# Optimization experiments

Hardware: AMD Instinct MI355X
Metric: run time of the kernel (lower is better)

## Reference

```python
import jax, jax.numpy as jnp
import numpy as np

HEADS = 8


def setup_inputs() -> dict:
    key = jax.random.key(0)
    ks = jax.random.split(key, 5)
    B, C, H, W = 2, 256, 48, 48
    s = 0.02
    return {
        "ct": jax.random.normal(ks[0], (B, C, H, W), jnp.float32),
        "us": jax.random.normal(ks[1], (B, C, H, W), jnp.float32),
        "w_qkv_ct": jax.random.normal(ks[2], (3 * C, C), jnp.float32) * s,
        "w_qkv_us": jax.random.normal(ks[3], (3 * C, C), jnp.float32) * s,
        "w_proj": jax.random.normal(ks[4], (C, 2 * C), jnp.float32) * s,
        "b_proj": jnp.zeros((C,), jnp.float32),
    }


def _heads_view(x, B, H, W):
    # [B, C, H, W] -> [B, heads, HW, dh]
    C = x.shape[1]
    return x.reshape(B, HEADS, C // HEADS, H * W).transpose(0, 1, 3, 2)


def _cross_attn(q, k, v, scale):
    # q,k,v: [B, heads, HW, dh]
    attn = jax.nn.softmax(jnp.einsum("bhnd,bhmd->bhnm", q, k) * scale, axis=-1)
    return jnp.einsum("bhnm,bhmd->bhnd", attn, v)


def reference(ct, us, w_qkv_ct, w_qkv_us, w_proj, b_proj):
    B, C, H, W = ct.shape
    dh = C // HEADS
    scale = dh ** (-0.5)

    # 1x1 convs as channel GEMMs
    qkv1 = jnp.einsum("oc,bchw->bohw", w_qkv_ct, ct)
    qkv2 = jnp.einsum("oc,bchw->bohw", w_qkv_us, us)
    q1, k1, v1 = jnp.split(qkv1, 3, axis=1)
    q2, k2, v2 = jnp.split(qkv2, 3, axis=1)

    # CT queries attend to US keys/values
    o1 = _cross_attn(_heads_view(q1, B, H, W), _heads_view(k2, B, H, W),
                     _heads_view(v2, B, H, W), scale)
    # US queries attend to CT keys/values
    o2 = _cross_attn(_heads_view(q2, B, H, W), _heads_view(k1, B, H, W),
                     _heads_view(v1, B, H, W), scale)

    # [B, heads, HW, dh] -> [B, C, H, W]
    out1 = o1.transpose(0, 1, 3, 2).reshape(B, C, H, W)
    out2 = o2.transpose(0, 1, 3, 2).reshape(B, C, H, W)

    fused = jnp.concatenate([ct + out1, us + out2], axis=1)
    return jnp.einsum("oc,bchw->bohw", w_proj, fused) + b_proj[None, :, None, None]
```

## Files before the change

### kernel.cpp

```cpp
#include <hip/hip_runtime.h>
#include <hip/hip_bf16.h>
#include <hip/hip_cooperative_groups.h>
#include <math.h>

namespace cg = cooperative_groups;

#define HW   2304
#define CCH  256

#define QSCALE 0.25504368686637270f

typedef short short8 __attribute__((ext_vector_type(8)));
typedef float f32x4  __attribute__((ext_vector_type(4)));

__device__ inline unsigned short f2bf(float f) {
    union { float f; unsigned u; } v; v.f = f;
    unsigned r = v.u + 0x7FFF + ((v.u >> 16) & 1);
    return (unsigned short)(r >> 16);
}
__device__ inline unsigned pkbf2(float a, float b) {
    float2 f; f.x = a; f.y = b;
    union { __hip_bfloat162 h; unsigned u; } c;
    c.h = __float22bfloat162_rn(f);
    return c.u;
}
__device__ inline unsigned pktrunc(float a, float b) {
    return __builtin_amdgcn_perm(__builtin_bit_cast(unsigned, b),
                                 __builtin_bit_cast(unsigned, a), 0x07060302u);
}

__device__ __forceinline__ int xswz(int i, int chunk) {
    return (i & 7) * chunk + (i >> 3);
}


__device__ __forceinline__ void prep_unit(
    int u, int t,
    const float* __restrict__ ct, const float* __restrict__ us,
    const float* __restrict__ w1, const float* __restrict__ w2,
    const float* __restrict__ w3,
    unsigned short* __restrict__ xT,
    unsigned short* __restrict__ wb1, unsigned short* __restrict__ wb2,
    unsigned short* __restrict__ w3b,
    unsigned short* __restrict__ Ts )
{
    if (u >= 576) {
        const int v_ = u - 576;
        int z, base;
        if (v_ < 192)      { z = 0; base = v_ * 1024; }
        else if (v_ < 384) { z = 1; base = (v_ - 192) * 1024; }
        else               { z = 2; base = (v_ - 384) * 1024; }
        const float* s = (z == 0) ? w1 : (z == 1) ? w2 : w3;
        unsigned short* d = (z == 0) ? wb1 : (z == 1) ? wb2 : w3b;
        const int i = base + t * 4;
        const float4 v4 = *(const float4*)&s[i];
        const float sc = (z < 2 && i < 65536) ? QSCALE : 1.f;
        uint2 p; p.x = pkbf2(v4.x * sc, v4.y * sc); p.y = pkbf2(v4.z * sc, v4.w * sc);
        *(uint2*)&d[i] = p;
        return;
    }
    const int pt = u % 36, rest = u / 36, ctile = rest & 3, z = rest >> 2;
    const float* __restrict__ src = ((z >> 1) ? us : ct) + (size_t)(z & 1) * CCH * HW;
    unsigned short* __restrict__ dst = xT + (size_t)z * HW * 256;
    const int p0 = pt * 64, c0 = ctile * 64;
    __syncthreads();
#pragma unroll
    for (int r = 0; r < 4; r++) {
        const int c = (t >> 4) + 16 * r;
        const float4 v4 = *(const float4*)&src[(size_t)(c0 + c) * HW + p0 + (t & 15) * 4];
        Ts[((t & 15) * 4 + 0) * 72 + c] = f2bf(v4.x);
        Ts[((t & 15) * 4 + 1) * 72 + c] = f2bf(v4.y);
        Ts[((t & 15) * 4 + 2) * 72 + c] = f2bf(v4.z);
        Ts[((t & 15) * 4 + 3) * 72 + c] = f2bf(v4.w);
    }
    __syncthreads();
    const int p = t >> 2, c8 = (t & 3) * 16;
    const short8 a  = *(const short8*)&Ts[p * 72 + c8];
    const short8 b8 = *(const short8*)&Ts[p * 72 + c8 + 8];
    *(short8*)&dst[(size_t)(p0 + p) * 256 + c0 + c8]     = a;
    *(short8*)&dst[(size_t)(p0 + p) * 256 + c0 + c8 + 8] = b8;
}

__device__ __forceinline__ void qkv_unit(
    int ptile, int otile, int z, int t,
    const unsigned short* __restrict__ xT,
    const unsigned short* __restrict__ wb1, const unsigned short* __restrict__ wb2,
    unsigned short* __restrict__ qkvT1, unsigned short* __restrict__ qkvT2,
    unsigned short* __restrict__ vdm1,  unsigned short* __restrict__ vdm2,
    unsigned short* __restrict__ Ws, unsigned short* __restrict__ Xs)
{
    const int inp = z >> 1, b = z & 1;
    const unsigned short* __restrict__ X = xT + (size_t)(inp * 2 + b) * HW * 256;
    const unsigned short* __restrict__ W = inp ? wb2 : wb1;
    unsigned short* __restrict__ qT = (inp ? qkvT2 : qkvT1) + (size_t)b * HW * 512;
    unsigned short* __restrict__ vd = (inp ? vdm2 : vdm1) + (size_t)b * CCH * HW;
    const int p0 = ptile * 64, o0 = otile * 64;
    const int w = t >> 6, lane = t & 63, quad = lane >> 4, m = lane & 15;
    const int sr = t >> 3, sc = t & 7;

    f32x4 acc[4] = {{0,0,0,0},{0,0,0,0},{0,0,0,0},{0,0,0,0}};

    short8 wv0 = *(const short8*)&W[(size_t)(o0 + sr) * 256 + sc * 8];
    short8 wv1 = *(const short8*)&W[(size_t)(o0 + 32 + sr) * 256 + sc * 8];
    short8 xv0 = *(const short8*)&X[(size_t)(p0 + sr) * 256 + sc * 8];
    short8 xv1 = *(const short8*)&X[(size_t)(p0 + 32 + sr) * 256 + sc * 8];

    for (int k0 = 0; k0 < 256; k0 += 64) {
        __syncthreads();
        *(short8*)&Ws[sr * 72 + sc * 8] = wv0;
        *(short8*)&Ws[(32 + sr) * 72 + sc * 8] = wv1;
        *(short8*)&Xs[sr * 72 + sc * 8] = xv0;
        *(short8*)&Xs[(32 + sr) * 72 + sc * 8] = xv1;
        __syncthreads();
        const int kn = k0 + 64;
        if (kn < 256) {
            wv0 = *(const short8*)&W[(size_t)(o0 + sr) * 256 + kn + sc * 8];
            wv1 = *(const short8*)&W[(size_t)(o0 + 32 + sr) * 256 + kn + sc * 8];
            xv0 = *(const short8*)&X[(size_t)(p0 + sr) * 256 + kn + sc * 8];
            xv1 = *(const short8*)&X[(size_t)(p0 + 32 + sr) * 256 + kn + sc * 8];
        }
#pragma unroll
        for (int kc2 = 0; kc2 < 2; kc2++) {
            const short8 af = *(const short8*)&Ws[(w * 16 + m) * 72 + kc2 * 32 + quad * 8];
#pragma unroll
            for (int pg = 0; pg < 4; pg++) {
                const short8 bf = *(const short8*)&Xs[(pg * 16 + m) * 72 + kc2 * 32 + quad * 8];
                acc[pg] = __builtin_amdgcn_mfma_f32_16x16x32_bf16(af, bf, acc[pg], 0, 0, 0);
            }
        }
    }
    __syncthreads();
    if (o0 < 512) {
#pragma unroll
        for (int pg = 0; pg < 4; pg++) {
            uint2 pk; pk.x = pkbf2(acc[pg][0], acc[pg][1]); pk.y = pkbf2(acc[pg][2], acc[pg][3]);
            *(uint2*)&Ws[(pg * 16 + m) * 72 + w * 16 + quad * 4] = pk;
        }
        __syncthreads();
        const int pr = t >> 2, cc = t & 3;
        const uint4 d0 = *(const uint4*)&Ws[pr * 72 + cc * 16];
        const uint4 d1 = *(const uint4*)&Ws[pr * 72 + cc * 16 + 8];
        *(uint4*)&qT[(size_t)(p0 + pr) * 512 + o0 + cc * 16]     = d0;
        *(uint4*)&qT[(size_t)(p0 + pr) * 512 + o0 + cc * 16 + 8] = d1;
    } else {
#pragma unroll
        for (int pg = 0; pg < 4; pg++)
#pragma unroll
            for (int r = 0; r < 4; r++)
                Ws[(w * 16 + quad * 4 + r) * 72 + pg * 16 + m] = f2bf(acc[pg][r]);
        __syncthreads();
        const int dr = t >> 2, cc = t & 3;
        const uint4 d0 = *(const uint4*)&Ws[dr * 72 + cc * 16];
        const uint4 d1 = *(const uint4*)&Ws[dr * 72 + cc * 16 + 8];
        *(uint4*)&vd[(size_t)(o0 - 512 + dr) * HW + p0 + cc * 16]     = d0;
        *(uint4*)&vd[(size_t)(o0 - 512 + dr) * HW + p0 + cc * 16 + 8] = d1;
    }
    __syncthreads();
}

__device__ __forceinline__ void attn_unit(
    int ptile, int dir, int b, int h, int t,
    const unsigned short* __restrict__ qkvT1, const unsigned short* __restrict__ qkvT2,
    const unsigned short* __restrict__ vdm1,  const unsigned short* __restrict__ vdm2,
    const float* __restrict__ ct, const float* __restrict__ us,
    unsigned short* __restrict__ fusedT,
    unsigned short* __restrict__ Ks , unsigned short* __restrict__ Vs )
{
    const unsigned short* __restrict__ Qt = (dir ? qkvT2 : qkvT1) + (size_t)b * HW * 512;
    const unsigned short* __restrict__ Kt = (dir ? qkvT1 : qkvT2) + (size_t)b * HW * 512
                                            + 256 + h * 32;
    const unsigned short* __restrict__ Vd = (dir ? vdm1 : vdm2) + ((size_t)b * CCH + h * 32) * HW;
    const float* __restrict__ src = (dir ? us : ct) + ((size_t)b * CCH + h * 32) * HW;

    const int w = t >> 6, lane = t & 63, quad = lane >> 4, m = lane & 15;
    const int kj0 = t >> 2, kcs = t & 3;
    const int pcK = kcs ^ (((kj0 >> 1) & 1) | (((kj0 >> 3) & 1) << 1));
    const int vr0 = t >> 4, vcs = t & 15;
    const int g2m = ((m >> 1) & 1) | (((m >> 2) & 1) << 1);
    const unsigned short* __restrict__ ksb =
        &Ks[((m >> 2) * 8 + (m & 3)) * 32 + (quad ^ g2m) * 8];
    const unsigned short* __restrict__ vsb = &Vs[m * 136 + quad * 8];
    const short ONE = (short)0x3F80;
    const short8 ones = {ONE,ONE,ONE,ONE,ONE,ONE,ONE,ONE};

    const int pq = ptile * 64 + w * 16 + m;
    const short8 qf = *(const short8*)&Qt[(size_t)pq * 512 + h * 32 + quad * 8];

    f32x4 acc0 = {0,0,0,0}, acc1 = {0,0,0,0}, accl = {0,0,0,0};

    short8 ka = *(const short8*)&Kt[(size_t)kj0 * 512 + kcs * 8];
    short8 kb = *(const short8*)&Kt[(size_t)(kj0 + 64) * 512 + kcs * 8];
    short8 va = *(const short8*)&Vd[(size_t)vr0 * HW + vcs * 8];
    short8 vb = *(const short8*)&Vd[(size_t)(vr0 + 16) * HW + vcs * 8];

    for (int j0 = 0; j0 < HW; j0 += 128) {
        __syncthreads();
        *(short8*)&Ks[kj0 * 32 + pcK * 8] = ka;
        *(short8*)&Ks[(kj0 + 64) * 32 + pcK * 8] = kb;
        *(short8*)&Vs[vr0 * 136 + vcs * 8] = va;
        *(short8*)&Vs[(vr0 + 16) * 136 + vcs * 8] = vb;
        __syncthreads();

        const int jn = j0 + 128;
        if (jn < HW) {
            ka = *(const short8*)&Kt[(size_t)(jn + kj0) * 512 + kcs * 8];
            kb = *(const short8*)&Kt[(size_t)(jn + kj0 + 64) * 512 + kcs * 8];
            va = *(const short8*)&Vd[(size_t)vr0 * HW + jn + vcs * 8];
            vb = *(const short8*)&Vd[(size_t)(vr0 + 16) * HW + jn + vcs * 8];
        }

        uint4 pw4[4];
#pragma unroll
        for (int f = 0; f < 8; f++) {
            const short8 kf = *(const short8*)(ksb + ((f >> 1) * 32 + (f & 1) * 4) * 32);
            const f32x4 z = {0,0,0,0};
            const f32x4 S = __builtin_amdgcn_mfma_f32_16x16x32_bf16(kf, qf, z, 0, 0, 0);
            const float e0 = __builtin_amdgcn_exp2f(S[0]);
            const float e1 = __builtin_amdgcn_exp2f(S[1]);
            const float e2 = __builtin_amdgcn_exp2f(S[2]);
            const float e3 = __builtin_amdgcn_exp2f(S[3]);
            if ((f & 1) == 0) { pw4[f >> 1].x = pktrunc(e0, e1); pw4[f >> 1].y = pktrunc(e2, e3); }
            else              { pw4[f >> 1].z = pktrunc(e0, e1); pw4[f >> 1].w = pktrunc(e2, e3); }
        }
#pragma unroll
        for (int kt = 0; kt < 4; kt++) {
            const short8 pf = __builtin_bit_cast(short8, pw4[kt]);
            const short8 vf0 = *(const short8*)(vsb + kt * 32);
            const short8 vf1 = *(const short8*)(vsb + 16 * 136 + kt * 32);
            acc0 = __builtin_amdgcn_mfma_f32_16x16x32_bf16(vf0, pf, acc0, 0, 0, 0);
            acc1 = __builtin_amdgcn_mfma_f32_16x16x32_bf16(vf1, pf, acc1, 0, 0, 0);
            accl = __builtin_amdgcn_mfma_f32_16x16x32_bf16(ones, pf, accl, 0, 0, 0);
        }
    }

    const float inv = 1.f / accl[0];
    const int cb = dir * 256 + h * 32, d0 = quad * 4;
    unsigned short* __restrict__ fT = fusedT + ((size_t)b * HW + pq) * 512 + cb + d0;
    uint2 s0, s1;
    s0.x = pkbf2(acc0[0] * inv + src[(size_t)(d0 + 0) * HW + pq],
                 acc0[1] * inv + src[(size_t)(d0 + 1) * HW + pq]);
    s0.y = pkbf2(acc0[2] * inv + src[(size_t)(d0 + 2) * HW + pq],
                 acc0[3] * inv + src[(size_t)(d0 + 3) * HW + pq]);
    s1.x = pkbf2(acc1[0] * inv + src[(size_t)(16 + d0 + 0) * HW + pq],
                 acc1[1] * inv + src[(size_t)(16 + d0 + 1) * HW + pq]);
    s1.y = pkbf2(acc1[2] * inv + src[(size_t)(16 + d0 + 2) * HW + pq],
                 acc1[3] * inv + src[(size_t)(16 + d0 + 3) * HW + pq]);
    *(uint2*)&fT[0]  = s0;
    *(uint2*)&fT[16] = s1;
    __syncthreads();
}

__device__ __forceinline__ void proj_unit(
    int ptile, int otile, int t,
    const unsigned short* __restrict__ w3b, const unsigned short* __restrict__ fusedT,
    const float* __restrict__ bias, float* __restrict__ out,
    unsigned short* __restrict__ Ws, unsigned short* __restrict__ Xs)
{
    const int p0 = ptile * 64, o0 = otile * 64;
    const int w = t >> 6, lane = t & 63, quad = lane >> 4, m = lane & 15;
    const int sr = t >> 3, sc = t & 7;

    f32x4 acc[4] = {{0,0,0,0},{0,0,0,0},{0,0,0,0},{0,0,0,0}};

    short8 wv0 = *(const short8*)&w3b[(size_t)(o0 + sr) * 512 + sc * 8];
    short8 wv1 = *(const short8*)&w3b[(size_t)(o0 + 32 + sr) * 512 + sc * 8];
    short8 xv0 = *(const short8*)&fusedT[(size_t)(p0 + sr) * 512 + sc * 8];
    short8 xv1 = *(const short8*)&fusedT[(size_t)(p0 + 32 + sr) * 512 + sc * 8];

    for (int k0 = 0; k0 < 512; k0 += 64) {
        __syncthreads();
        *(short8*)&Ws[sr * 72 + sc * 8] = wv0;
        *(short8*)&Ws[(32 + sr) * 72 + sc * 8] = wv1;
        *(short8*)&Xs[sr * 72 + sc * 8] = xv0;
        *(short8*)&Xs[(32 + sr) * 72 + sc * 8] = xv1;
        __syncthreads();
        const int kn = k0 + 64;
        if (kn < 512) {
            wv0 = *(const short8*)&w3b[(size_t)(o0 + sr) * 512 + kn + sc * 8];
            wv1 = *(const short8*)&w3b[(size_t)(o0 + 32 + sr) * 512 + kn + sc * 8];
            xv0 = *(const short8*)&fusedT[(size_t)(p0 + sr) * 512 + kn + sc * 8];
            xv1 = *(const short8*)&fusedT[(size_t)(p0 + 32 + sr) * 512 + kn + sc * 8];
        }
#pragma unroll
        for (int kc2 = 0; kc2 < 2; kc2++) {
            const short8 af = *(const short8*)&Ws[(w * 16 + m) * 72 + kc2 * 32 + quad * 8];
#pragma unroll
            for (int pg = 0; pg < 4; pg++) {
                const short8 bf = *(const short8*)&Xs[(pg * 16 + m) * 72 + kc2 * 32 + quad * 8];
                acc[pg] = __builtin_amdgcn_mfma_f32_16x16x32_bf16(af, bf, acc[pg], 0, 0, 0);
            }
        }
    }
    const int b = (p0 >= HW) ? 1 : 0;
    const int pl0 = p0 - b * HW;
    float* __restrict__ ob = out + (size_t)b * CCH * HW;
    float b4[4];
#pragma unroll
    for (int r = 0; r < 4; r++) b4[r] = bias[o0 + w * 16 + quad * 4 + r];
#pragma unroll
    for (int pg = 0; pg < 4; pg++)
#pragma unroll
        for (int r = 0; r < 4; r++)
            ob[(size_t)(o0 + w * 16 + quad * 4 + r) * HW + pl0 + pg * 16 + m]
                = acc[pg][r] + b4[r];
}

__global__ __launch_bounds__(256, 5) void fused_k(
    const float* __restrict__ ct, const float* __restrict__ us,
    const float* __restrict__ w1, const float* __restrict__ w2,
    const float* __restrict__ w3, const float* __restrict__ bias,
    float* __restrict__ out,
    unsigned short* __restrict__ xT,
    unsigned short* __restrict__ wb1, unsigned short* __restrict__ wb2,
    unsigned short* __restrict__ w3b,
    unsigned short* __restrict__ qkvT1, unsigned short* __restrict__ qkvT2,
    unsigned short* __restrict__ vdm1,  unsigned short* __restrict__ vdm2,
    unsigned short* __restrict__ fusedT)
{
    cg::grid_group grid = cg::this_grid();
    __shared__ __align__(16) unsigned short smem[9216];
    const int t = threadIdx.x, nb = gridDim.x;

    for (int u = blockIdx.x; u < 1088; u += nb)
        prep_unit(u, t, ct, us, w1, w2, w3, xT, wb1, wb2, w3b, smem);
    __threadfence();
    grid.sync();

    for (int i = blockIdx.x; i < 1728; i += nb) {
        const int u = xswz(i, 216);
        const int ptile = u % 36, rest = u / 36;
        qkv_unit(ptile, rest % 12, rest / 12, t, xT, wb1, wb2,
                 qkvT1, qkvT2, vdm1, vdm2, smem, smem + 4608);
    }
    __threadfence();
    grid.sync();

    {
        const int u = xswz(blockIdx.x, 144);
        const int ptile = u % 36, rest = u / 36;
        attn_unit(ptile, rest >> 4, (rest >> 3) & 1, rest & 7, t,
                  qkvT1, qkvT2, vdm1, vdm2, ct, us, fusedT, smem, smem + 4096);
    }
    __threadfence();
    grid.sync();

    if (blockIdx.x < 288) {
        const int u = xswz(blockIdx.x, 36);
        proj_unit(u % 72, u / 72, t, w3b, fusedT, bias, out,
                  smem, smem + 4608);
    }
}

__global__ __launch_bounds__(256, 4) void prep_k(
    const float* __restrict__ ct, const float* __restrict__ us,
    const float* __restrict__ w1, const float* __restrict__ w2,
    const float* __restrict__ w3,
    unsigned short* __restrict__ xT,
    unsigned short* __restrict__ b1, unsigned short* __restrict__ b2,
    unsigned short* __restrict__ b3)
{
    __shared__ __align__(16) unsigned short Ts[64 * 72];
    prep_unit(blockIdx.x, threadIdx.x, ct, us, w1, w2, w3, xT, b1, b2, b3, Ts);
}

__global__ __launch_bounds__(256, 4) void qkv_k(
    const unsigned short* __restrict__ xT,
    const unsigned short* __restrict__ wb1, const unsigned short* __restrict__ wb2,
    unsigned short* __restrict__ qkvT1, unsigned short* __restrict__ qkvT2,
    unsigned short* __restrict__ vdm1,  unsigned short* __restrict__ vdm2)
{
    __shared__ __align__(16) unsigned short Ws[64 * 72];
    __shared__ __align__(16) unsigned short Xs[64 * 72];
    qkv_unit(blockIdx.x, blockIdx.y, blockIdx.z, threadIdx.x,
             xT, wb1, wb2, qkvT1, qkvT2, vdm1, vdm2, Ws, Xs);
}

__global__ __launch_bounds__(256, 5) void attn_k(
    const unsigned short* __restrict__ qkvT1, const unsigned short* __restrict__ qkvT2,
    const unsigned short* __restrict__ vdm1,  const unsigned short* __restrict__ vdm2,
    const float* __restrict__ ct, const float* __restrict__ us,
    unsigned short* __restrict__ fusedT)
{
    __shared__ __align__(16) unsigned short Ks[128 * 32];
    __shared__ __align__(16) unsigned short Vs[32 * 136];
    attn_unit(blockIdx.x, blockIdx.z, blockIdx.y >> 3, blockIdx.y & 7, threadIdx.x,
              qkvT1, qkvT2, vdm1, vdm2, ct, us, fusedT, Ks, Vs);
}

__global__ __launch_bounds__(256, 4) void proj_k(
    const unsigned short* __restrict__ w3b, const unsigned short* __restrict__ fusedT,
    const float* __restrict__ bias, float* __restrict__ out)
{
    __shared__ __align__(16) unsigned short Ws[64 * 72];
    __shared__ __align__(16) unsigned short Xs[64 * 72];
    proj_unit(blockIdx.x, blockIdx.y, threadIdx.x, w3b, fusedT, bias, out, Ws, Xs);
}

extern "C" void kernel_launch(void* const* d_in, const int* in_sizes, int n_in,
                              void* d_out, int out_size, void* d_ws, size_t ws_size,
                              hipStream_t stream)
{
    const float* ct       = (const float*)d_in[0];
    const float* us       = (const float*)d_in[1];
    const float* w_qkv_ct = (const float*)d_in[2];
    const float* w_qkv_us = (const float*)d_in[3];
    const float* w_proj   = (const float*)d_in[4];
    const float* b_proj   = (const float*)d_in[5];
    float* out = (float*)d_out;

    unsigned short* wb1   = (unsigned short*)d_ws;
    unsigned short* wb2   = wb1 + (size_t)768 * 256;
    unsigned short* w3b   = wb2 + (size_t)768 * 256;
    unsigned short* xT    = w3b + (size_t)256 * 512;
    unsigned short* qkvT1 = xT    + (size_t)4 * HW * 256;
    unsigned short* qkvT2 = qkvT1 + (size_t)2 * HW * 512;
    unsigned short* vdm1  = qkvT2 + (size_t)2 * HW * 512;
    unsigned short* vdm2  = vdm1  + (size_t)2 * CCH * HW;
    unsigned short* fusedT= vdm2  + (size_t)2 * CCH * HW;

    int dev = 0, coop = 0, occ = 0;
    bool did_coop = false;
    if (hipGetDevice(&dev) == hipSuccess &&
        hipDeviceGetAttribute(&coop, hipDeviceAttributeCooperativeLaunch, dev) == hipSuccess &&
        coop &&
        hipOccupancyMaxActiveBlocksPerMultiprocessor(&occ, fused_k, 256, 0) == hipSuccess &&
        occ >= 5)
    {
        void* args[] = {
            (void*)&ct, (void*)&us, (void*)&w_qkv_ct, (void*)&w_qkv_us,
            (void*)&w_proj, (void*)&b_proj, (void*)&out,
            (void*)&xT, (void*)&wb1, (void*)&wb2, (void*)&w3b,
            (void*)&qkvT1, (void*)&qkvT2, (void*)&vdm1, (void*)&vdm2, (void*)&fusedT
        };
        did_coop = (hipLaunchCooperativeKernel((const void*)fused_k, dim3(1152), dim3(256),
                                               args, 0, stream) == hipSuccess);
    }
    if (!did_coop) {
        prep_k<<<dim3(1088), 256, 0, stream>>>(ct, us, w_qkv_ct, w_qkv_us, w_proj,
                                               xT, wb1, wb2, w3b);
        qkv_k <<<dim3(36, 12, 4), 256, 0, stream>>>(xT, wb1, wb2, qkvT1, qkvT2, vdm1, vdm2);
        attn_k<<<dim3(36, 16, 2), 256, 0, stream>>>(qkvT1, qkvT2, vdm1, vdm2, ct, us, fusedT);
        proj_k<<<dim3(72, 4), 256, 0, stream>>>(w3b, fusedT, b_proj, out);
    }
}
```

Measured before the change: 126.0 us.

## Process two query tiles per attention wave and swizzle prep transpose LDS

```diff
diff --git a/kernel.cpp b/kernel.cpp
--- a/kernel.cpp
+++ b/kernel.cpp
@@ -63,20 +63,23 @@
     const float* __restrict__ src = ((z >> 1) ? us : ct) + (size_t)(z & 1) * CCH * HW;
     unsigned short* __restrict__ dst = xT + (size_t)z * HW * 256;
     const int p0 = pt * 64, c0 = ctile * 64;
+    const int m = t & 15, ms = (m & 7) << 3;
     __syncthreads();
 #pragma unroll
     for (int r = 0; r < 4; r++) {
         const int c = (t >> 4) + 16 * r;
-        const float4 v4 = *(const float4*)&src[(size_t)(c0 + c) * HW + p0 + (t & 15) * 4];
-        Ts[((t & 15) * 4 + 0) * 72 + c] = f2bf(v4.x);
-        Ts[((t & 15) * 4 + 1) * 72 + c] = f2bf(v4.y);
-        Ts[((t & 15) * 4 + 2) * 72 + c] = f2bf(v4.z);
-        Ts[((t & 15) * 4 + 3) * 72 + c] = f2bf(v4.w);
+        const float4 v4 = *(const float4*)&src[(size_t)(c0 + c) * HW + p0 + m * 4];
+        const int cs = c ^ ms;
+        Ts[(m * 4 + 0) * 72 + cs] = f2bf(v4.x);
+        Ts[(m * 4 + 1) * 72 + cs] = f2bf(v4.y);
+        Ts[(m * 4 + 2) * 72 + cs] = f2bf(v4.z);
+        Ts[(m * 4 + 3) * 72 + cs] = f2bf(v4.w);
     }
     __syncthreads();
     const int p = t >> 2, c8 = (t & 3) * 16;
-    const short8 a  = *(const short8*)&Ts[p * 72 + c8];
-    const short8 b8 = *(const short8*)&Ts[p * 72 + c8 + 8];
+    const int es = ((p >> 2) & 7) << 3;
+    const short8 a  = *(const short8*)&Ts[p * 72 + (c8 ^ es)];
+    const short8 b8 = *(const short8*)&Ts[p * 72 + ((c8 + 8) ^ es)];
     *(short8*)&dst[(size_t)(p0 + p) * 256 + c0 + c8]     = a;
     *(short8*)&dst[(size_t)(p0 + p) * 256 + c0 + c8 + 8] = b8;
 }
@@ -183,10 +186,12 @@
     const short ONE = (short)0x3F80;
     const short8 ones = {ONE,ONE,ONE,ONE,ONE,ONE,ONE,ONE};
 
-    const int pq = ptile * 64 + w * 16 + m;
-    const short8 qf = *(const short8*)&Qt[(size_t)pq * 512 + h * 32 + quad * 8];
-
-    f32x4 acc0 = {0,0,0,0}, acc1 = {0,0,0,0}, accl = {0,0,0,0};
+    const int pqA = ptile * 128 + w * 32 + m;
+    const short8 qfA = *(const short8*)&Qt[(size_t)pqA * 512 + h * 32 + quad * 8];
+    const short8 qfB = *(const short8*)&Qt[(size_t)(pqA + 16) * 512 + h * 32 + quad * 8];
+
+    f32x4 acc0A = {0,0,0,0}, acc1A = {0,0,0,0}, acclA = {0,0,0,0};
+    f32x4 acc0B = {0,0,0,0}, acc1B = {0,0,0,0}, acclB = {0,0,0,0};
 
     short8 ka = *(const short8*)&Kt[(size_t)kj0 * 512 + kcs * 8];
     short8 kb = *(const short8*)&Kt[(size_t)(kj0 + 64) * 512 + kcs * 8];
@@ -209,44 +214,76 @@
             vb = *(const short8*)&Vd[(size_t)(vr0 + 16) * HW + jn + vcs * 8];
         }
 
-        uint4 pw4[4];
+        uint4 pwA[4], pwB[4];
 #pragma unroll
         for (int f = 0; f < 8; f++) {
             const short8 kf = *(const short8*)(ksb + ((f >> 1) * 32 + (f & 1) * 4) * 32);
             const f32x4 z = {0,0,0,0};
-            const f32x4 S = __builtin_amdgcn_mfma_f32_16x16x32_bf16(kf, qf, z, 0, 0, 0);
-            const float e0 = __builtin_amdgcn_exp2f(S[0]);
-            const float e1 = __builtin_amdgcn_exp2f(S[1]);
-            const float e2 = __builtin_amdgcn_exp2f(S[2]);
-            const float e3 = __builtin_amdgcn_exp2f(S[3]);
-            if ((f & 1) == 0) { pw4[f >> 1].x = pktrunc(e0, e1); pw4[f >> 1].y = pktrunc(e2, e3); }
-            else              { pw4[f >> 1].z = pktrunc(e0, e1); pw4[f >> 1].w = pktrunc(e2, e3); }
+            const f32x4 SA = __builtin_amdgcn_mfma_f32_16x16x32_bf16(kf, qfA, z, 0, 0, 0);
+            const f32x4 SB = __builtin_amdgcn_mfma_f32_16x16x32_bf16(kf, qfB, z, 0, 0, 0);
+            const float a0 = __builtin_amdgcn_exp2f(SA[0]);
+            const float a1 = __builtin_amdgcn_exp2f(SA[1]);
+            const float a2 = __builtin_amdgcn_exp2f(SA[2]);
+            const float a3 = __builtin_amdgcn_exp2f(SA[3]);
+            const float b0 = __builtin_amdgcn_exp2f(SB[0]);
+            const float b1 = __builtin_amdgcn_exp2f(SB[1]);
+            const float b2 = __builtin_amdgcn_exp2f(SB[2]);
+            const float b3 = __builtin_amdgcn_exp2f(SB[3]);
+            if ((f & 1) == 0) {
+                pwA[f >> 1].x = pktrunc(a0, a1); pwA[f >> 1].y = pktrunc(a2, a3);
+                pwB[f >> 1].x = pktrunc(b0, b1); pwB[f >> 1].y = pktrunc(b2, b3);
+            } else {
+                pwA[f >> 1].z = pktrunc(a0, a1); pwA[f >> 1].w = pktrunc(a2, a3);
+                pwB[f >> 1].z = pktrunc(b0, b1); pwB[f >> 1].w = pktrunc(b2, b3);
+            }
         }
 #pragma unroll
         for (int kt = 0; kt < 4; kt++) {
-            const short8 pf = __builtin_bit_cast(short8, pw4[kt]);
+            const short8 pfA = __builtin_bit_cast(short8, pwA[kt]);
+            const short8 pfB = __builtin_bit_cast(short8, pwB[kt]);
             const short8 vf0 = *(const short8*)(vsb + kt * 32);
             const short8 vf1 = *(const short8*)(vsb + 16 * 136 + kt * 32);
-            acc0 = __builtin_amdgcn_mfma_f32_16x16x32_bf16(vf0, pf, acc0, 0, 0, 0);
-            acc1 = __builtin_amdgcn_mfma_f32_16x16x32_bf16(vf1, pf, acc1, 0, 0, 0);
-            accl = __builtin_amdgcn_mfma_f32_16x16x32_bf16(ones, pf, accl, 0, 0, 0);
-        }
-    }
-
-    const float inv = 1.f / accl[0];
+            acc0A = __builtin_amdgcn_mfma_f32_16x16x32_bf16(vf0, pfA, acc0A, 0, 0, 0);
+            acc1A = __builtin_amdgcn_mfma_f32_16x16x32_bf16(vf1, pfA, acc1A, 0, 0, 0);
+            acclA = __builtin_amdgcn_mfma_f32_16x16x32_bf16(ones, pfA, acclA, 0, 0, 0);
+            acc0B = __builtin_amdgcn_mfma_f32_16x16x32_bf16(vf0, pfB, acc0B, 0, 0, 0);
+            acc1B = __builtin_amdgcn_mfma_f32_16x16x32_bf16(vf1, pfB, acc1B, 0, 0, 0);
+            acclB = __builtin_amdgcn_mfma_f32_16x16x32_bf16(ones, pfB, acclB, 0, 0, 0);
+        }
+    }
+
     const int cb = dir * 256 + h * 32, d0 = quad * 4;
-    unsigned short* __restrict__ fT = fusedT + ((size_t)b * HW + pq) * 512 + cb + d0;
-    uint2 s0, s1;
-    s0.x = pkbf2(acc0[0] * inv + src[(size_t)(d0 + 0) * HW + pq],
-                 acc0[1] * inv + src[(size_t)(d0 + 1) * HW + pq]);
-    s0.y = pkbf2(acc0[2] * inv + src[(size_t)(d0 + 2) * HW + pq],
-                 acc0[3] * inv + src[(size_t)(d0 + 3) * HW + pq]);
-    s1.x = pkbf2(acc1[0] * inv + src[(size_t)(16 + d0 + 0) * HW + pq],
-                 acc1[1] * inv + src[(size_t)(16 + d0 + 1) * HW + pq]);
-    s1.y = pkbf2(acc1[2] * inv + src[(size_t)(16 + d0 + 2) * HW + pq],
-                 acc1[3] * inv + src[(size_t)(16 + d0 + 3) * HW + pq]);
-    *(uint2*)&fT[0]  = s0;
-    *(uint2*)&fT[16] = s1;
+    {
+        const float inv = 1.f / acclA[0];
+        unsigned short* __restrict__ fT = fusedT + ((size_t)b * HW + pqA) * 512 + cb + d0;
+        uint2 s0, s1;
+        s0.x = pkbf2(acc0A[0] * inv + src[(size_t)(d0 + 0) * HW + pqA],
+                     acc0A[1] * inv + src[(size_t)(d0 + 1) * HW + pqA]);
+        s0.y = pkbf2(acc0A[2] * inv + src[(size_t)(d0 + 2) * HW + pqA],
+                     acc0A[3] * inv + src[(size_t)(d0 + 3) * HW + pqA]);
+        s1.x = pkbf2(acc1A[0] * inv + src[(size_t)(16 + d0 + 0) * HW + pqA],
+                     acc1A[1] * inv + src[(size_t)(16 + d0 + 1) * HW + pqA]);
+        s1.y = pkbf2(acc1A[2] * inv + src[(size_t)(16 + d0 + 2) * HW + pqA],
+                     acc1A[3] * inv + src[(size_t)(16 + d0 + 3) * HW + pqA]);
+        *(uint2*)&fT[0]  = s0;
+        *(uint2*)&fT[16] = s1;
+    }
+    {
+        const int pqB = pqA + 16;
+        const float inv = 1.f / acclB[0];
+        unsigned short* __restrict__ fT = fusedT + ((size_t)b * HW + pqB) * 512 + cb + d0;
+        uint2 s0, s1;
+        s0.x = pkbf2(acc0B[0] * inv + src[(size_t)(d0 + 0) * HW + pqB],
+                     acc0B[1] * inv + src[(size_t)(d0 + 1) * HW + pqB]);
+        s0.y = pkbf2(acc0B[2] * inv + src[(size_t)(d0 + 2) * HW + pqB],
+                     acc0B[3] * inv + src[(size_t)(d0 + 3) * HW + pqB]);
+        s1.x = pkbf2(acc1B[0] * inv + src[(size_t)(16 + d0 + 0) * HW + pqB],
+                     acc1B[1] * inv + src[(size_t)(16 + d0 + 1) * HW + pqB]);
+        s1.y = pkbf2(acc1B[2] * inv + src[(size_t)(16 + d0 + 2) * HW + pqB],
+                     acc1B[3] * inv + src[(size_t)(16 + d0 + 3) * HW + pqB]);
+        *(uint2*)&fT[0]  = s0;
+        *(uint2*)&fT[16] = s1;
+    }
     __syncthreads();
 }
 
@@ -305,7 +342,7 @@
                 = acc[pg][r] + b4[r];
 }
 
-__global__ __launch_bounds__(256, 5) void fused_k(
+__global__ __launch_bounds__(256, 3) void fused_k(
     const float* __restrict__ ct, const float* __restrict__ us,
     const float* __restrict__ w1, const float* __restrict__ w2,
     const float* __restrict__ w3, const float* __restrict__ bias,
@@ -336,8 +373,8 @@
     grid.sync();
 
     {
-        const int u = xswz(blockIdx.x, 144);
-        const int ptile = u % 36, rest = u / 36;
+        const int u = xswz(blockIdx.x, 72);
+        const int ptile = u % 18, rest = u / 18;
         attn_unit(ptile, rest >> 4, (rest >> 3) & 1, rest & 7, t,
                   qkvT1, qkvT2, vdm1, vdm2, ct, us, fusedT, smem, smem + 4096);
     }
@@ -375,7 +412,7 @@
              xT, wb1, wb2, qkvT1, qkvT2, vdm1, vdm2, Ws, Xs);
 }
 
-__global__ __launch_bounds__(256, 5) void attn_k(
+__global__ __launch_bounds__(256, 3) void attn_k(
     const unsigned short* __restrict__ qkvT1, const unsigned short* __restrict__ qkvT2,
     const unsigned short* __restrict__ vdm1,  const unsigned short* __restrict__ vdm2,
     const float* __restrict__ ct, const float* __restrict__ us,
@@ -424,7 +461,7 @@
         hipDeviceGetAttribute(&coop, hipDeviceAttributeCooperativeLaunch, dev) == hipSuccess &&
         coop &&
         hipOccupancyMaxActiveBlocksPerMultiprocessor(&occ, fused_k, 256, 0) == hipSuccess &&
-        occ >= 5)
+        occ >= 3)
     {
         void* args[] = {
             (void*)&ct, (void*)&us, (void*)&w_qkv_ct, (void*)&w_qkv_us,
@@ -432,14 +469,14 @@
             (void*)&xT, (void*)&wb1, (void*)&wb2, (void*)&w3b,
             (void*)&qkvT1, (void*)&qkvT2, (void*)&vdm1, (void*)&vdm2, (void*)&fusedT
         };
-        did_coop = (hipLaunchCooperativeKernel((const void*)fused_k, dim3(1152), dim3(256),
+        did_coop = (hipLaunchCooperativeKernel((const void*)fused_k, dim3(576), dim3(256),
                                                args, 0, stream) == hipSuccess);
     }
     if (!did_coop) {
         prep_k<<<dim3(1088), 256, 0, stream>>>(ct, us, w_qkv_ct, w_qkv_us, w_proj,
                                                xT, wb1, wb2, w3b);
         qkv_k <<<dim3(36, 12, 4), 256, 0, stream>>>(xT, wb1, wb2, qkvT1, qkvT2, vdm1, vdm2);
-        attn_k<<<dim3(36, 16, 2), 256, 0, stream>>>(qkvT1, qkvT2, vdm1, vdm2, ct, us, fusedT);
+        attn_k<<<dim3(18, 16, 2), 256, 0, stream>>>(qkvT1, qkvT2, vdm1, vdm2, ct, us, fusedT);
         proj_k<<<dim3(72, 4), 256, 0, stream>>>(w3b, fusedT, b_proj, out);
     }
 }
```

Result: no change. 124.7 us (-1.0%).
